# Performance work log

Hardware: AMD Instinct MI355X
Metric: run time of the kernel (lower is better)

The kernel has to match this reference:

```python
import jax, jax.numpy as jnp
import numpy as np

N = 50000      # nodes
E = 800000     # edges (before self-loops)
F_IN = 128     # in_dim
H = 8          # heads
C = 16         # out_dim per head
NEG_SLOPE = 0.2
EPS = 1e-5


def setup_inputs() -> dict:
    key = jax.random.key(0)
    ks = jax.random.split(key, 8)
    x = jax.random.normal(ks[0], (N, F_IN), dtype=jnp.float32)
    edge_index = jax.random.randint(ks[1], (2, E), 0, N, dtype=jnp.int64)
    # GAT linear weight (xavier-ish scale), stored as [F_IN, H*C]
    W_gat = jax.random.normal(ks[2], (F_IN, H * C), dtype=jnp.float32) * 0.1
    att_src = jax.random.normal(ks[3], (H, C), dtype=jnp.float32) * 0.1
    att_dst = jax.random.normal(ks[4], (H, C), dtype=jnp.float32) * 0.1
    bias_gat = jnp.zeros((H * C,), dtype=jnp.float32)
    W_skip = jax.random.normal(ks[5], (F_IN, H * C), dtype=jnp.float32) * 0.1
    gamma = jnp.ones((H * C,), dtype=jnp.float32)
    beta = jnp.zeros((H * C,), dtype=jnp.float32)
    return {"x": x, "edge_index": edge_index, "W_gat": W_gat,
            "att_src": att_src, "att_dst": att_dst, "bias_gat": bias_gat,
            "W_skip": W_skip, "gamma": gamma, "beta": beta}


def reference(x, edge_index, W_gat, att_src, att_dst, bias_gat, W_skip, gamma, beta):
    # PyG GATConv default: add self-loops
    loop = jnp.arange(N, dtype=edge_index.dtype)
    src = jnp.concatenate([edge_index[0], loop])  # [E+N]
    dst = jnp.concatenate([edge_index[1], loop])  # [E+N]

    h = (x @ W_gat).reshape(N, H, C)              # [N,H,C]
    a_src = jnp.sum(h * att_src, axis=-1)          # [N,H]
    a_dst = jnp.sum(h * att_dst, axis=-1)          # [N,H]

    e = jax.nn.leaky_relu(a_src[src] + a_dst[dst], NEG_SLOPE)   # [E+N,H]
    # segment softmax over destination nodes
    e_max = jax.ops.segment_max(e, dst, num_segments=N)         # [N,H]
    e_exp = jnp.exp(e - e_max[dst])
    denom = jax.ops.segment_sum(e_exp, dst, num_segments=N)     # [N,H]
    alpha = e_exp / denom[dst]                                   # [E+N,H]

    msg = alpha[:, :, None] * h[src]                             # [E+N,H,C]
    gat_out = jax.ops.segment_sum(msg, dst, num_segments=N)     # [N,H,C]
    gat_out = gat_out.reshape(N, H * C) + bias_gat

    skip_out = x @ W_skip                                        # [N,H*C]
    z = gat_out + 0.1 * skip_out

    mu = jnp.mean(z, axis=-1, keepdims=True)
    var = jnp.mean((z - mu) ** 2, axis=-1, keepdims=True)
    z = (z - mu) * jax.lax.rsqrt(var + EPS) * gamma + beta
    return jax.nn.elu(z)  # dropout is identity in eval mode
```

## Files before the change

kernel.cpp:

```cpp
#include <hip/hip_runtime.h>
#include <hip/hip_bf16.h>

#define N_NODES 50000
#define N_EDGES 800000
#define F_IN    128
#define HC      128
#define NR      8
#define RSZ     6250
#define NCH     32
#define CHSZ    25000
#define NP      50048

#define LOG2E   1.4426950408889634f

typedef __attribute__((ext_vector_type(8))) short bf16x8;
typedef __attribute__((ext_vector_type(4))) float f32x4;

__device__ __forceinline__ float bf2f(unsigned int u16) {
    return __uint_as_float(u16 << 16);
}
__device__ __forceinline__ unsigned int f2bf2(float lo, float hi) {
    unsigned int r;
    asm("v_cvt_pk_bf16_f32 %0, %1, %2" : "=v"(r) : "v"(lo), "v"(hi));
    return r;
}
__device__ __forceinline__ float exp2_hw(float x) {
    float r;
    asm("v_exp_f32 %0, %1" : "=v"(r) : "v"(x));
    return r;
}

__device__ __forceinline__ void linear_block(
    int lin, int tid, int* smem,
    const float* __restrict__ x, const unsigned short* __restrict__ Bfrag,
    const float* __restrict__ att_s, const float* __restrict__ att_d,
    const float* __restrict__ bias,
    unsigned short* __restrict__ h_bf, unsigned int* __restrict__ z0b,
    float* __restrict__ a_src, float* __restrict__ a_dst)
{
    unsigned short* sA = (unsigned short*)smem;
    const int lane = tid & 63;
    const int w = tid >> 6;
    const int nbase = lin * 64;

#pragma unroll
    for (int it = 0; it < 4; it++) {
        const int p = it * 256 + tid;
        const int node = p >> 4;
        const int kg = p & 15;
        const int gn = nbase + node;
        float v[8];
        if (gn < N_NODES) {
            float4 u0 = *(const float4*)(x + (size_t)gn * F_IN + kg * 8);
            float4 u1 = *(const float4*)(x + (size_t)gn * F_IN + kg * 8 + 4);
            v[0] = u0.x; v[1] = u0.y; v[2] = u0.z; v[3] = u0.w;
            v[4] = u1.x; v[5] = u1.y; v[6] = u1.z; v[7] = u1.w;
        } else {
#pragma unroll
            for (int j = 0; j < 8; j++) v[j] = 0.f;
        }
        const int mt = node >> 4, lm = node & 15;
        const int kq = kg >> 2, quad = kg & 3;
        uint4 pk;
        pk.x = f2bf2(v[0], v[1]);
        pk.y = f2bf2(v[2], v[3]);
        pk.z = f2bf2(v[4], v[5]);
        pk.w = f2bf2(v[6], v[7]);
        *(uint4*)(sA + ((size_t)((mt * 4 + kq) * 64 + quad * 16 + lm)) * 8) = pk;
    }
    __syncthreads();

    const bf16x8* Bf = (const bf16x8*)Bfrag;
    f32x4 acc[4][4];
#pragma unroll
    for (int mt = 0; mt < 4; mt++)
#pragma unroll
        for (int nt = 0; nt < 4; nt++)
            acc[mt][nt] = (f32x4){0.f, 0.f, 0.f, 0.f};

#pragma unroll
    for (int kq = 0; kq < 4; kq++) {
        bf16x8 aF[4], bF[4];
#pragma unroll
        for (int nt = 0; nt < 4; nt++)
            bF[nt] = Bf[(size_t)(((w * 4 + nt) * 4 + kq) * 64 + lane)];
#pragma unroll
        for (int mt = 0; mt < 4; mt++)
            aF[mt] = *(const bf16x8*)(sA + ((size_t)((mt * 4 + kq) * 64 + lane)) * 8);
#pragma unroll
        for (int mt = 0; mt < 4; mt++)
#pragma unroll
            for (int nt = 0; nt < 4; nt++)
                acc[mt][nt] = __builtin_amdgcn_mfma_f32_16x16x32_bf16(
                    aF[mt], bF[nt], acc[mt][nt], 0, 0, 0);
    }

    __syncthreads();

    const int row4 = (lane >> 4) * 4;
    const int cl = lane & 15;
    unsigned int* hls = (unsigned int*)smem;

    if (w < 2) {
#pragma unroll
        for (int mt = 0; mt < 4; mt++) {
#pragma unroll
            for (int nt = 0; nt < 4; nt++) {
                const int cc = w * 64 + nt * 16 + cl;
                f32x4 d = acc[mt][nt];
#pragma unroll
                for (int rr = 0; rr < 4; rr++) {
                    const float oth = __shfl_xor(d[rr], 1);
                    const unsigned int pk = f2bf2(d[rr], oth);
                    if ((cl & 1) == 0) {
                        const int nl = mt * 16 + row4 + rr;
                        hls[nl * 68 + (cc >> 1)] = pk;
                    }
                }
            }
        }
    } else {
#pragma unroll
        for (int mt = 0; mt < 4; mt++) {
#pragma unroll
            for (int nt = 0; nt < 4; nt++) {
                const int cz = (w - 2) * 64 + nt * 16 + cl;
                f32x4 d = acc[mt][nt];
                const float bv = bias[cz];
#pragma unroll
                for (int rr = 0; rr < 4; rr++) {
                    const int gn = nbase + mt * 16 + row4 + rr;
                    const float val = 0.1f * d[rr] + bv;
                    const float oth = __shfl_xor(val, 1);
                    const unsigned int pk = f2bf2(val, oth);
                    if ((cl & 1) == 0 && gn < N_NODES)
                        z0b[(size_t)gn * 64 + (cz >> 1)] = pk;
                }
            }
        }
    }
    __syncthreads();

    {
        const int row = tid >> 2, q = tid & 3;
        const int gn = nbase + row;
        if (gn < N_NODES) {
            const unsigned int* hr = hls + row * 68 + q * 16;
            uint4 v0 = *(const uint4*)(hr);
            uint4 v1 = *(const uint4*)(hr + 4);
            uint4 v2 = *(const uint4*)(hr + 8);
            uint4 v3 = *(const uint4*)(hr + 12);
            uint4* hout = (uint4*)((unsigned int*)h_bf + (size_t)gn * 64 + q * 16);
            hout[0] = v0; hout[1] = v1; hout[2] = v2; hout[3] = v3;

            const unsigned int u[16] = {v0.x, v0.y, v0.z, v0.w,
                                        v1.x, v1.y, v1.z, v1.w,
                                        v2.x, v2.y, v2.z, v2.w,
                                        v3.x, v3.y, v3.z, v3.w};
            const int c0 = q * 32;
            const float4* as4 = (const float4*)(att_s + c0);
            const float4* ad4 = (const float4*)(att_d + c0);
            float ds0 = 0.f, dd0 = 0.f, ds1 = 0.f, dd1 = 0.f;
#pragma unroll
            for (int j = 0; j < 4; j++) {
                const float4 sa = as4[j], da = ad4[j];
                float l0 = bf2f(u[2 * j] & 0xffffu),     h0v = bf2f(u[2 * j] >> 16);
                float l1 = bf2f(u[2 * j + 1] & 0xffffu), h1v = bf2f(u[2 * j + 1] >> 16);
                ds0 += l0 * sa.x + h0v * sa.y + l1 * sa.z + h1v * sa.w;
                dd0 += l0 * da.x + h0v * da.y + l1 * da.z + h1v * da.w;
                const float4 sb = as4[4 + j], db = ad4[4 + j];
                float l2 = bf2f(u[8 + 2 * j] & 0xffffu),     h2v = bf2f(u[8 + 2 * j] >> 16);
                float l3 = bf2f(u[8 + 2 * j + 1] & 0xffffu), h3v = bf2f(u[8 + 2 * j + 1] >> 16);
                ds1 += l2 * sb.x + h2v * sb.y + l3 * sb.z + h3v * sb.w;
                dd1 += l2 * db.x + h2v * db.y + l3 * db.z + h3v * db.w;
            }
            const int hh = 2 * q;
            a_src[gn * 8 + hh]     = ds0 * LOG2E;
            a_src[gn * 8 + hh + 1] = ds1 * LOG2E;
            a_dst[gn * 8 + hh]     = dd0 * LOG2E;
            a_dst[gn * 8 + hh + 1] = dd1 * LOG2E;
        }
    }
}

__global__ __launch_bounds__(256) void k_pack(
    const float* __restrict__ Wg, const float* __restrict__ Ws,
    unsigned short* __restrict__ Bfrag)
{
    const int g = blockIdx.x * 256 + threadIdx.x;
    if (g < 4096) {
        const int lane = g & 63;
        const int kq = (g >> 6) & 3;
        const int nt = g >> 8;
        const int cc = nt * 16 + (lane & 15);
        const int kbase = kq * 32 + (lane >> 4) * 8;
        const float* Wsel = (cc < 128) ? (Wg + cc) : (Ws + cc - 128);
        unsigned int pk[4];
#pragma unroll
        for (int p = 0; p < 4; p++) {
            const float v0 = Wsel[(size_t)(kbase + 2 * p) * HC];
            const float v1 = Wsel[(size_t)(kbase + 2 * p + 1) * HC];
            pk[p] = f2bf2(v0, v1);
        }
        *(uint4*)(Bfrag + (size_t)g * 8) = make_uint4(pk[0], pk[1], pk[2], pk[3]);
    }
}

__global__ __launch_bounds__(256) void k_hl(
    const int* __restrict__ dst, int* __restrict__ part,
    const float* __restrict__ x, const unsigned short* __restrict__ Bfrag,
    const float* __restrict__ att_s, const float* __restrict__ att_d,
    const float* __restrict__ bias,
    unsigned short* __restrict__ h_bf, unsigned int* __restrict__ z0b,
    float* __restrict__ a_src, float* __restrict__ a_dst)
{
    __shared__ __align__(16) int smem[RSZ];
    const int bid = blockIdx.x;
    const int tid = threadIdx.x;
    if (bid < 256) {
        const int r = bid & 7, c = bid >> 3;
        const int nb = r * RSZ;
        for (int i = tid; i < RSZ; i += 256) smem[i] = 0;
        __syncthreads();
        const int4* d4 = (const int4*)(dst + c * CHSZ);
        for (int i = tid; i < CHSZ / 4; i += 256) {
            const int4 v = d4[i];
            int b;
            b = v.x - nb; if ((unsigned)b < (unsigned)RSZ) atomicAdd(&smem[b], 1);
            b = v.y - nb; if ((unsigned)b < (unsigned)RSZ) atomicAdd(&smem[b], 1);
            b = v.z - nb; if ((unsigned)b < (unsigned)RSZ) atomicAdd(&smem[b], 1);
            b = v.w - nb; if ((unsigned)b < (unsigned)RSZ) atomicAdd(&smem[b], 1);
        }
        __syncthreads();
        for (int i = tid; i < RSZ; i += 256)
            part[(size_t)c * NP + nb + i] = smem[i];
        return;
    }
    linear_block(bid - 256, tid, smem, x, Bfrag, att_s, att_d, bias,
                 h_bf, z0b, a_src, a_dst);
}

__global__ __launch_bounds__(256) void k_sl(
    int* __restrict__ part, int* __restrict__ counts,
    int* __restrict__ row_start, int* __restrict__ bsum,
    const float* __restrict__ x, const unsigned short* __restrict__ Bfrag,
    const float* __restrict__ att_s, const float* __restrict__ att_d,
    const float* __restrict__ bias,
    unsigned short* __restrict__ h_bf, unsigned int* __restrict__ z0b,
    float* __restrict__ a_src, float* __restrict__ a_dst)
{
    __shared__ __align__(16) int smem[RSZ];
    const int bid = blockIdx.x;
    const int tid = threadIdx.x;
    if (bid < 49) {
        int* s = smem;
        const int base = bid * 1024 + tid * 4;
        int v[4]; int t = 0;
#pragma unroll
        for (int j = 0; j < 4; j++) {
            const int idx = base + j;
            if (idx < N_NODES) {
                int run = 0;
#pragma unroll
                for (int c = 0; c < NCH; c++) {
                    int* p = part + (size_t)c * NP + idx;
                    const int q = *p;
                    *p = run;
                    run += q;
                }
                counts[idx] = run;
                v[j] = run + 1;
            } else v[j] = 0;
            t += v[j];
        }
        s[tid] = t;
        __syncthreads();
        for (int off = 1; off < 256; off <<= 1) {
            int add = (tid >= off) ? s[tid - off] : 0;
            __syncthreads();
            s[tid] += add;
            __syncthreads();
        }
        int excl = s[tid] - t;
#pragma unroll
        for (int j = 0; j < 4; j++) {
            const int idx = base + j;
            if (idx < N_NODES) row_start[idx] = excl;
            excl += v[j];
        }
        if (tid == 255) bsum[bid] = s[255];
        return;
    }
    linear_block(260 + (bid - 49), tid, smem, x, Bfrag, att_s, att_d, bias,
                 h_bf, z0b, a_src, a_dst);
}

__global__ __launch_bounds__(256) void k_scanC(
    int* __restrict__ row_start, const int* __restrict__ bsum,
    const int* __restrict__ counts, int* __restrict__ csr)
{
    __shared__ int soff;
    const int tid = threadIdx.x;
    if (tid < 64) {
        const int tgt = blockIdx.x >> 2;
        int v = (tid < 49 && tid < tgt) ? bsum[tid] : 0;
#pragma unroll
        for (int off = 1; off < 64; off <<= 1) v += __shfl_xor(v, off);
        if (tid == 0) soff = v;
    }
    __syncthreads();
    const int i = blockIdx.x * 256 + tid;
    if (i < N_NODES) {
        const int rs = row_start[i] + soff;
        row_start[i] = rs;
        csr[rs + counts[i]] = i;
    }
}

__global__ __launch_bounds__(256) void k_lf(
    const int* __restrict__ src, const int* __restrict__ dst,
    const int* __restrict__ row_start, const int* __restrict__ part,
    int* __restrict__ csr,
    const float* __restrict__ x, const unsigned short* __restrict__ Bfrag,
    const float* __restrict__ att_s, const float* __restrict__ att_d,
    const float* __restrict__ bias,
    unsigned short* __restrict__ h_bf, unsigned int* __restrict__ z0b,
    float* __restrict__ a_src, float* __restrict__ a_dst)
{
    __shared__ __align__(16) int smem[RSZ];
    const int bid = blockIdx.x;
    const int tid = threadIdx.x;
    int lin;
    if (bid < 512) {
        const int c = bid >> 4, pos = bid & 15;
        if (pos < 8) {
            const int r = pos;
            const int nb = r * RSZ;
            for (int b = tid; b < RSZ; b += 256)
                smem[b] = row_start[nb + b] + part[(size_t)c * NP + nb + b];
            __syncthreads();
            const int4* d4 = (const int4*)(dst + c * CHSZ);
            const int4* s4 = (const int4*)(src + c * CHSZ);
            for (int i = tid; i < CHSZ / 4; i += 256) {
                const int4 dv = d4[i];
                const int4 sv = s4[i];
                int b;
                b = dv.x - nb; if ((unsigned)b < (unsigned)RSZ) csr[atomicAdd(&smem[b], 1)] = sv.x;
                b = dv.y - nb; if ((unsigned)b < (unsigned)RSZ) csr[atomicAdd(&smem[b], 1)] = sv.y;
                b = dv.z - nb; if ((unsigned)b < (unsigned)RSZ) csr[atomicAdd(&smem[b], 1)] = sv.z;
                b = dv.w - nb; if ((unsigned)b < (unsigned)RSZ) csr[atomicAdd(&smem[b], 1)] = sv.w;
            }
            return;
        }
        lin = 521 + c * 8 + (pos - 8);
    } else {
        lin = 777 + (bid - 512);
    }
    linear_block(lin, tid, smem, x, Bfrag, att_s, att_d, bias,
                 h_bf, z0b, a_src, a_dst);
}

__global__ __launch_bounds__(256) void k_agg(
    const unsigned int* __restrict__ h32,
    const unsigned int* __restrict__ z0b,
    const float* __restrict__ a_src, const float* __restrict__ a_dst,
    const int* __restrict__ row_start, const int* __restrict__ counts,
    const int* __restrict__ csr,
    const float* __restrict__ gamma, const float* __restrict__ beta,
    float* __restrict__ out)
{
    const int tid = threadIdx.x;
    const int lane = tid & 63;
    const int n = blockIdx.x * 4 + (tid >> 6);
    const int head = lane >> 3;

    const float adn = a_dst[n * 8 + head];
    const int rs  = __builtin_amdgcn_readfirstlane(row_start[n]);
    const int cnt = __builtin_amdgcn_readfirstlane(counts[n]) + 1;

    const char* h8 = (const char*)h32;
    const char* a8 = (const char*)a_src;
    const unsigned int hoff = (unsigned)(lane << 2);
    const unsigned int aoff = (unsigned)(head << 2);

    float d_acc = 0.f, a0 = 0.f, a1 = 0.f;
    const int nfull = cnt & ~7;
    int i = 0;
    for (; i < nfull; i += 8) {
        int s[8]; float ae[8]; unsigned int hp[8];
#pragma unroll
        for (int j = 0; j < 8; j++) s[j] = csr[rs + i + j];
#pragma unroll
        for (int j = 0; j < 8; j++)
            ae[j] = *(const float*)(a8 + ((unsigned)(s[j] << 5) | aoff));
#pragma unroll
        for (int j = 0; j < 8; j++)
            hp[j] = *(const unsigned int*)(h8 + ((unsigned)(s[j] << 8) | hoff));
#pragma unroll
        for (int j = 0; j < 8; j++) {
            float e = ae[j] + adn;
            e = fmaxf(e, 0.2f * e);
            const float wgt = exp2_hw(e);
            d_acc += wgt;
            a0 += wgt * bf2f(hp[j] & 0xffffu);
            a1 += wgt * bf2f(hp[j] >> 16);
        }
    }
    if (i < cnt) {
        int s[8]; float ae[8], mk[8]; unsigned int hp[8];
#pragma unroll
        for (int j = 0; j < 8; j++) {
            const int e = i + j;
            const int ec = (e < cnt) ? e : (cnt - 1);
            mk[j] = (e < cnt) ? 1.f : 0.f;
            s[j] = csr[rs + ec];
        }
#pragma unroll
        for (int j = 0; j < 8; j++)
            ae[j] = *(const float*)(a8 + ((unsigned)(s[j] << 5) | aoff));
#pragma unroll
        for (int j = 0; j < 8; j++)
            hp[j] = *(const unsigned int*)(h8 + ((unsigned)(s[j] << 8) | hoff));
#pragma unroll
        for (int j = 0; j < 8; j++) {
            float e = ae[j] + adn;
            e = fmaxf(e, 0.2f * e);
            const float wgt = exp2_hw(e) * mk[j];
            d_acc += wgt;
            a0 += wgt * bf2f(hp[j] & 0xffffu);
            a1 += wgt * bf2f(hp[j] >> 16);
        }
    }
    const float inv = 1.0f / d_acc;
    const unsigned int zp = z0b[(size_t)n * 64 + lane];
    float y0 = a0 * inv + bf2f(zp & 0xffffu);
    float y1 = a1 * inv + bf2f(zp >> 16);

    float ss = y0 + y1;
#pragma unroll
    for (int off = 1; off < 64; off <<= 1) ss += __shfl_xor(ss, off);
    const float mu = ss * (1.0f / 128.0f);
    const float d0 = y0 - mu, d1 = y1 - mu;
    float vs = d0 * d0 + d1 * d1;
#pragma unroll
    for (int off = 1; off < 64; off <<= 1) vs += __shfl_xor(vs, off);
    const float rstd = rsqrtf(vs * (1.0f / 128.0f) + 1e-5f);

    const float2 gv = *(const float2*)(gamma + lane * 2);
    const float2 bv = *(const float2*)(beta + lane * 2);
    float o0 = d0 * rstd * gv.x + bv.x;
    float o1 = d1 * rstd * gv.y + bv.y;
    o0 = (o0 > 0.f) ? o0 : (__expf(o0) - 1.0f);
    o1 = (o1 > 0.f) ? o1 : (__expf(o1) - 1.0f);

    *(float2*)(out + (size_t)n * HC + lane * 2) = make_float2(o0, o1);
}

extern "C" void kernel_launch(void* const* d_in, const int* in_sizes, int n_in,
                              void* d_out, int out_size, void* d_ws, size_t ws_size,
                              hipStream_t stream) {
    const float* x   = (const float*)d_in[0];
    const int*   ei  = (const int*)d_in[1];
    const float* Wg  = (const float*)d_in[2];
    const float* as_ = (const float*)d_in[3];
    const float* ad_ = (const float*)d_in[4];
    const float* bg  = (const float*)d_in[5];
    const float* Wsk = (const float*)d_in[6];
    const float* gm  = (const float*)d_in[7];
    const float* bt  = (const float*)d_in[8];
    float* out = (float*)d_out;

    char* wsb = (char*)d_ws;
    unsigned short* h_bf  = (unsigned short*)wsb;
    unsigned int*   z0b   = (unsigned int*)(wsb + 12800000);
    float*          a_src = (float*)(wsb + 25600000);
    float*          a_dst = (float*)(wsb + 27200000);
    unsigned short* Bfrag = (unsigned short*)(wsb + 28800000);
    int*   counts = (int*)(wsb + 28865536);
    int*   row_st = (int*)(wsb + 29065728);
    int*   bsum   = (int*)(wsb + 29265920);
    int*   csr    = (int*)(wsb + 29266944);
    int*   part   = (int*)(wsb + 32666944);

    const int* src = ei;
    const int* dst = ei + N_EDGES;

    k_pack <<<16, 256, 0, stream>>>(Wg, Wsk, Bfrag);
    k_hl   <<<516, 256, 0, stream>>>(dst, part, x, Bfrag, as_, ad_, bg,
                                     h_bf, z0b, a_src, a_dst);
    k_sl   <<<310, 256, 0, stream>>>(part, counts, row_st, bsum,
                                     x, Bfrag, as_, ad_, bg,
                                     h_bf, z0b, a_src, a_dst);
    k_scanC<<<196, 256, 0, stream>>>(row_st, bsum, counts, csr);
    k_lf   <<<517, 256, 0, stream>>>(src, dst, row_st, part, csr,
                                     x, Bfrag, as_, ad_, bg,
                                     h_bf, z0b, a_src, a_dst);
    k_agg  <<<N_NODES / 4, 256, 0, stream>>>((const unsigned int*)h_bf, z0b,
                                             a_src, a_dst, row_st, counts, csr,
                                             gm, bt, out);
}
```

Measured before the change: 205.0 us.

## Fold block-offset scan into CSR fill kernel and unroll aggregation by 16

Removes the separate k_scanC launch. Each fill block now computes the exclusive prefix of the 49 block sums itself and adds it to the row starts it loads. The chunk-0 blocks also write the finalized row starts to a new row_fin buffer and place each self-loop entry. Separately, the aggregation kernel processes neighbors 16 at a time with an 8-wide step before the masked tail, giving more outstanding gathers per wave. This cuts one launch and one pass over row_start, at the cost of redundant small scans in every fill block and higher register pressure in k_agg.

```diff
diff --git a/kernel.cpp b/kernel.cpp
--- a/kernel.cpp
+++ b/kernel.cpp
@@ -295,32 +295,11 @@
                  h_bf, z0b, a_src, a_dst);
 }
 
-__global__ __launch_bounds__(256) void k_scanC(
-    int* __restrict__ row_start, const int* __restrict__ bsum,
-    const int* __restrict__ counts, int* __restrict__ csr)
-{
-    __shared__ int soff;
-    const int tid = threadIdx.x;
-    if (tid < 64) {
-        const int tgt = blockIdx.x >> 2;
-        int v = (tid < 49 && tid < tgt) ? bsum[tid] : 0;
-#pragma unroll
-        for (int off = 1; off < 64; off <<= 1) v += __shfl_xor(v, off);
-        if (tid == 0) soff = v;
-    }
-    __syncthreads();
-    const int i = blockIdx.x * 256 + tid;
-    if (i < N_NODES) {
-        const int rs = row_start[i] + soff;
-        row_start[i] = rs;
-        csr[rs + counts[i]] = i;
-    }
-}
-
 __global__ __launch_bounds__(256) void k_lf(
     const int* __restrict__ src, const int* __restrict__ dst,
     const int* __restrict__ row_start, const int* __restrict__ part,
-    int* __restrict__ csr,
+    const int* __restrict__ bsum, const int* __restrict__ counts,
+    int* __restrict__ row_fin, int* __restrict__ csr,
     const float* __restrict__ x, const unsigned short* __restrict__ Bfrag,
     const float* __restrict__ att_s, const float* __restrict__ att_d,
     const float* __restrict__ bias,
@@ -328,6 +307,7 @@
     float* __restrict__ a_src, float* __restrict__ a_dst)
 {
     __shared__ __align__(16) int smem[RSZ];
+    __shared__ int pbsum[64];
     const int bid = blockIdx.x;
     const int tid = threadIdx.x;
     int lin;
@@ -336,8 +316,32 @@
         if (pos < 8) {
             const int r = pos;
             const int nb = r * RSZ;
-            for (int b = tid; b < RSZ; b += 256)
-                smem[b] = row_start[nb + b] + part[(size_t)c * NP + nb + b];
+            if (tid < 64) {
+                const int val = (tid < 49) ? bsum[tid] : 0;
+                int v = val;
+#pragma unroll
+                for (int off = 1; off < 64; off <<= 1) {
+                    const int u = __shfl_up(v, off);
+                    if (tid >= off) v += u;
+                }
+                pbsum[tid] = v - val;
+            }
+            __syncthreads();
+            if (c == 0) {
+                for (int b = tid; b < RSZ; b += 256) {
+                    const int idx = nb + b;
+                    const int rsf = row_start[idx] + pbsum[idx >> 10];
+                    smem[b] = rsf + part[(size_t)c * NP + idx];
+                    row_fin[idx] = rsf;
+                    csr[rsf + counts[idx]] = idx;
+                }
+            } else {
+                for (int b = tid; b < RSZ; b += 256) {
+                    const int idx = nb + b;
+                    smem[b] = row_start[idx] + pbsum[idx >> 10]
+                            + part[(size_t)c * NP + idx];
+                }
+            }
             __syncthreads();
             const int4* d4 = (const int4*)(dst + c * CHSZ);
             const int4* s4 = (const int4*)(src + c * CHSZ);
@@ -364,7 +368,7 @@
     const unsigned int* __restrict__ h32,
     const unsigned int* __restrict__ z0b,
     const float* __restrict__ a_src, const float* __restrict__ a_dst,
-    const int* __restrict__ row_start, const int* __restrict__ counts,
+    const int* __restrict__ row_fin, const int* __restrict__ counts,
     const int* __restrict__ csr,
     const float* __restrict__ gamma, const float* __restrict__ beta,
     float* __restrict__ out)
@@ -375,7 +379,7 @@
     const int head = lane >> 3;
 
     const float adn = a_dst[n * 8 + head];
-    const int rs  = __builtin_amdgcn_readfirstlane(row_start[n]);
+    const int rs  = __builtin_amdgcn_readfirstlane(row_fin[n]);
     const int cnt = __builtin_amdgcn_readfirstlane(counts[n]) + 1;
 
     const char* h8 = (const char*)h32;
@@ -384,9 +388,29 @@
     const unsigned int aoff = (unsigned)(head << 2);
 
     float d_acc = 0.f, a0 = 0.f, a1 = 0.f;
-    const int nfull = cnt & ~7;
+    const int nfull16 = cnt & ~15;
     int i = 0;
-    for (; i < nfull; i += 8) {
+    for (; i < nfull16; i += 16) {
+        int s[16]; float ae[16]; unsigned int hp[16];
+#pragma unroll
+        for (int j = 0; j < 16; j++) s[j] = csr[rs + i + j];
+#pragma unroll
+        for (int j = 0; j < 16; j++)
+            ae[j] = *(const float*)(a8 + ((unsigned)(s[j] << 5) | aoff));
+#pragma unroll
+        for (int j = 0; j < 16; j++)
+            hp[j] = *(const unsigned int*)(h8 + ((unsigned)(s[j] << 8) | hoff));
+#pragma unroll
+        for (int j = 0; j < 16; j++) {
+            float e = ae[j] + adn;
+            e = fmaxf(e, 0.2f * e);
+            const float wgt = exp2_hw(e);
+            d_acc += wgt;
+            a0 += wgt * bf2f(hp[j] & 0xffffu);
+            a1 += wgt * bf2f(hp[j] >> 16);
+        }
+    }
+    if (i + 8 <= cnt) {
         int s[8]; float ae[8]; unsigned int hp[8];
 #pragma unroll
         for (int j = 0; j < 8; j++) s[j] = csr[rs + i + j];
@@ -405,6 +429,7 @@
             a0 += wgt * bf2f(hp[j] & 0xffffu);
             a1 += wgt * bf2f(hp[j] >> 16);
         }
+        i += 8;
     }
     if (i < cnt) {
         int s[8]; float ae[8], mk[8]; unsigned int hp[8];
@@ -481,6 +506,7 @@
     int*   bsum   = (int*)(wsb + 29265920);
     int*   csr    = (int*)(wsb + 29266944);
     int*   part   = (int*)(wsb + 32666944);
+    int*   row_fin= (int*)(wsb + 39073088);
 
     const int* src = ei;
     const int* dst = ei + N_EDGES;
@@ -491,11 +517,11 @@
     k_sl   <<<310, 256, 0, stream>>>(part, counts, row_st, bsum,
                                      x, Bfrag, as_, ad_, bg,
                                      h_bf, z0b, a_src, a_dst);
-    k_scanC<<<196, 256, 0, stream>>>(row_st, bsum, counts, csr);
-    k_lf   <<<517, 256, 0, stream>>>(src, dst, row_st, part, csr,
+    k_lf   <<<517, 256, 0, stream>>>(src, dst, row_st, part, bsum, counts,
+                                     row_fin, csr,
                                      x, Bfrag, as_, ad_, bg,
                                      h_bf, z0b, a_src, a_dst);
     k_agg  <<<N_NODES / 4, 256, 0, stream>>>((const unsigned int*)h_bf, z0b,
-                                             a_src, a_dst, row_st, counts, csr,
+                                             a_src, a_dst, row_fin, counts, csr,
                                              gm, bt, out);
 }
```

Measured after the change: 202.1 us. Within noise of the previous version (-1.4%).
